# Kernel tuning notes

Hardware: AMD Instinct MI355X
Metric: run time of the kernel (lower is better)

Reference implementation:

```python
import jax, jax.numpy as jnp
import numpy as np

N_NODES = 50000
N_EDGES = 800000
IN_DIM = 128
HID = 64      # per-head out channels of conv1 (concat=False)
HID2 = 32     # hidden_dim // 2, per-head out channels of conv2
HEADS = 4
LATENT = 32
NEG_SLOPE = 0.2


def gat_conv(x, W, a_src, a_dst, bias, src, dst, n_nodes):
    """PyG GATConv with concat=False (mean over heads). src->dst message flow."""
    H, C = a_src.shape
    xh = (x @ W).reshape(-1, H, C)                       # [N,H,C]
    al_s = jnp.einsum('nhc,hc->nh', xh, a_src)           # [N,H]
    al_d = jnp.einsum('nhc,hc->nh', xh, a_dst)           # [N,H]
    alpha = jax.nn.leaky_relu(al_s[src] + al_d[dst], NEG_SLOPE)  # [E,H]
    # segment softmax over incoming edges of each dst node
    amax = jax.ops.segment_max(alpha, dst, num_segments=n_nodes)
    ex = jnp.exp(alpha - amax[dst])
    denom = jax.ops.segment_sum(ex, dst, num_segments=n_nodes)
    coef = ex / (denom[dst] + 1e-16)                     # [E,H]
    msg = xh[src] * coef[:, :, None]                     # [E,H,C]
    out = jax.ops.segment_sum(msg, dst, num_segments=n_nodes)  # [N,H,C]
    return out.mean(axis=1) + bias                       # [N,C]


def setup_inputs() -> dict:
    key = jax.random.key(0)
    ks = jax.random.split(key, 16)
    s = lambda *sh: 1.0 / np.sqrt(sh[0])
    x = jax.random.normal(ks[0], (N_NODES, IN_DIM), dtype=jnp.float32)
    edge_index = jax.random.randint(ks[1], (2, N_EDGES), 0, N_NODES, dtype=jnp.int64)
    W1 = jax.random.normal(ks[2], (IN_DIM, HEADS * HID), dtype=jnp.float32) * s(IN_DIM)
    a_src1 = jax.random.normal(ks[3], (HEADS, HID), dtype=jnp.float32) * s(HID)
    a_dst1 = jax.random.normal(ks[4], (HEADS, HID), dtype=jnp.float32) * s(HID)
    b1 = jnp.zeros((HID,), dtype=jnp.float32)
    W2 = jax.random.normal(ks[5], (HID, HEADS * HID2), dtype=jnp.float32) * s(HID)
    a_src2 = jax.random.normal(ks[6], (HEADS, HID2), dtype=jnp.float32) * s(HID2)
    a_dst2 = jax.random.normal(ks[7], (HEADS, HID2), dtype=jnp.float32) * s(HID2)
    b2 = jnp.zeros((HID2,), dtype=jnp.float32)
    W_mu = jax.random.normal(ks[8], (HID2, LATENT), dtype=jnp.float32) * s(HID2)
    b_mu = jnp.zeros((LATENT,), dtype=jnp.float32)
    W_lv = jax.random.normal(ks[9], (HID2, LATENT), dtype=jnp.float32) * s(HID2)
    b_lv = jnp.zeros((LATENT,), dtype=jnp.float32)
    return {"x": x, "edge_index": edge_index, "W1": W1, "a_src1": a_src1,
            "a_dst1": a_dst1, "b1": b1, "W2": W2, "a_src2": a_src2,
            "a_dst2": a_dst2, "b2": b2, "W_mu": W_mu, "b_mu": b_mu,
            "W_lv": W_lv, "b_lv": b_lv}


def reference(x, edge_index, W1, a_src1, a_dst1, b1, W2, a_src2, a_dst2, b2,
              W_mu, b_mu, W_lv, b_lv):
    n = x.shape[0]
    loops = jnp.arange(n, dtype=edge_index.dtype)
    src = jnp.concatenate([edge_index[0], loops])  # PyG add_self_loops=True
    dst = jnp.concatenate([edge_index[1], loops])
    h = jax.nn.relu(gat_conv(x, W1, a_src1, a_dst1, b1, src, dst, n))
    h = jax.nn.relu(gat_conv(h, W2, a_src2, a_dst2, b2, src, dst, n))
    mu = h @ W_mu + b_mu
    logvar = h @ W_lv + b_lv
    return (mu, logvar)
```

## Files before the change

kernel.cpp:

```cpp
#include <hip/hip_runtime.h>
#include <hip/hip_fp16.h>

#define N_NODES 50000
#define N_EDGES 800000
#define IN_DIM  128
#define HID     64
#define HID2    32
#define HEADS   4
#define LATENT  32
#define NEG_SLOPE 0.2f
#define BINCAP  64

#define GB1   ((N_NODES + 63) / 64)
#define NBIN  ((N_EDGES + 255) / 256)

typedef _Float16 half8v __attribute__((ext_vector_type(8)));
typedef _Float16 half4v __attribute__((ext_vector_type(4)));
typedef float    float4v __attribute__((ext_vector_type(4)));

#define OFF_XH1H  ((size_t)0)
#define OFF_XH2H  ((size_t)0)
#define OFF_ALS2  ((size_t)8000000)
#define OFF_ALD2  ((size_t)8200000)
#define OFF_AGG1  ((size_t)8400000)
#define OFF_ALS1  ((size_t)11600000)
#define OFF_ALD1  ((size_t)11800000)
#define OFF_CUR   ((size_t)12000000)
#define OFF_ESRC  ((size_t)12050000)
#define OFF_W1TH  ((size_t)15250000)
#define OFF_W2TH  ((size_t)15266384)

#define NB_ZERO ((N_NODES + 255) / 256)

__device__ __forceinline__ float lrelu(float v) {
    return v > 0.f ? v : NEG_SLOPE * v;
}

__global__ void k_prep(const float* __restrict__ W1, const float* __restrict__ W2,
                       __half* __restrict__ w1t, __half* __restrict__ w2t,
                       int* __restrict__ cur) {
    if (blockIdx.x < 160) {
        const int t = blockIdx.x * 256 + threadIdx.x;
        if (t < 32768) {
            const int k = t >> 8, n = t & 255;
            w1t[n * IN_DIM + k] = __float2half(W1[t]);
        } else {
            const int t2 = t - 32768;
            const int k = t2 >> 7, n = t2 & 127;
            w2t[n * HID + k] = __float2half(W2[t2]);
        }
    } else {
        const int i = (blockIdx.x - 160) * 256 + threadIdx.x;
        if (i < N_NODES) cur[i] = 0;
    }
}

__global__ void k_gemm1_mfma(const float* __restrict__ x, const __half* __restrict__ w1t,
                             const float* __restrict__ as1, const float* __restrict__ ad1,
                             __half* __restrict__ xh1, float* __restrict__ als,
                             float* __restrict__ ald, const int* __restrict__ ei,
                             int* __restrict__ cur, int* __restrict__ esrc) {
    const int tid = threadIdx.x;
    if (blockIdx.x >= GB1) {
        const int e = (blockIdx.x - GB1) * 256 + tid;
        if (e < N_EDGES) {
            const int s = ei[e], dd = ei[N_EDGES + e];
            const int pos = atomicAdd(&cur[dd], 1);
            if (pos < BINCAP)
                __builtin_nontemporal_store(s, &esrc[(dd << 6) + pos]);
        }
        return;
    }
    __shared__ _Float16 xsh[64][136];
    __shared__ _Float16 wsh[64][136];
    const int m0 = blockIdx.x * 64;
#pragma unroll
    for (int i = 0; i < 8; i++) {
        const int f = tid + i * 256;
        const int r = f >> 5;
        const int k = (f & 31) * 4;
        const int gr = (m0 + r < N_NODES) ? (m0 + r) : (N_NODES - 1);
        const float4 xv = *(const float4*)(x + (size_t)gr * IN_DIM + k);
        half4v hv = { (_Float16)xv.x, (_Float16)xv.y, (_Float16)xv.z, (_Float16)xv.w };
        *(half4v*)&xsh[r][k] = hv;
    }
    const int w = tid >> 6, l = tid & 63;
    const int lr = l & 15;
    const int lk = (l >> 4) * 8;
    const int rbase = m0 + w * 16 + (l >> 4) * 4;
    for (int nb = 0; nb < 4; nb++) {
        const int n0 = nb * 64;
        __syncthreads();
#pragma unroll
        for (int i = 0; i < 4; i++) {
            const int u = tid + i * 256;
            const int r = u >> 4;
            const int k = (u & 15) * 8;
            *(half8v*)&wsh[r][k] = *(const half8v*)(w1t + (size_t)(n0 + r) * IN_DIM + k);
        }
        __syncthreads();
        float4v acc0 = {0.f,0.f,0.f,0.f}, acc1 = {0.f,0.f,0.f,0.f};
        float4v acc2 = {0.f,0.f,0.f,0.f}, acc3 = {0.f,0.f,0.f,0.f};
#pragma unroll
        for (int k0 = 0; k0 < IN_DIM; k0 += 32) {
            const half8v a  = *(const half8v*)&xsh[w * 16 + lr][k0 + lk];
            const half8v b0 = *(const half8v*)&wsh[ 0 + lr][k0 + lk];
            const half8v b1 = *(const half8v*)&wsh[16 + lr][k0 + lk];
            const half8v b2 = *(const half8v*)&wsh[32 + lr][k0 + lk];
            const half8v b3 = *(const half8v*)&wsh[48 + lr][k0 + lk];
            acc0 = __builtin_amdgcn_mfma_f32_16x16x32_f16(a, b0, acc0, 0, 0, 0);
            acc1 = __builtin_amdgcn_mfma_f32_16x16x32_f16(a, b1, acc1, 0, 0, 0);
            acc2 = __builtin_amdgcn_mfma_f32_16x16x32_f16(a, b2, acc2, 0, 0, 0);
            acc3 = __builtin_amdgcn_mfma_f32_16x16x32_f16(a, b3, acc3, 0, 0, 0);
        }
        const int cbase = n0 + lr;
#pragma unroll
        for (int r = 0; r < 4; r++) {
            const int node = rbase + r;
            if (node < N_NODES) {
                __half* p = xh1 + (size_t)node * (HEADS * HID) + cbase;
                p[0]  = __float2half(acc0[r]);
                p[16] = __float2half(acc1[r]);
                p[32] = __float2half(acc2[r]);
                p[48] = __float2half(acc3[r]);
            }
        }
        const int h = nb;
        const float a0 = as1[(h << 6) + lr +  0], a1 = as1[(h << 6) + lr + 16];
        const float a2 = as1[(h << 6) + lr + 32], a3 = as1[(h << 6) + lr + 48];
        const float d0 = ad1[(h << 6) + lr +  0], d1 = ad1[(h << 6) + lr + 16];
        const float d2 = ad1[(h << 6) + lr + 32], d3 = ad1[(h << 6) + lr + 48];
#pragma unroll
        for (int r = 0; r < 4; r++) {
            float ps = acc0[r] * a0 + acc1[r] * a1 + acc2[r] * a2 + acc3[r] * a3;
            float pd = acc0[r] * d0 + acc1[r] * d1 + acc2[r] * d2 + acc3[r] * d3;
            ps += __shfl_xor(ps, 1); pd += __shfl_xor(pd, 1);
            ps += __shfl_xor(ps, 2); pd += __shfl_xor(pd, 2);
            ps += __shfl_xor(ps, 4); pd += __shfl_xor(pd, 4);
            ps += __shfl_xor(ps, 8); pd += __shfl_xor(pd, 8);
            if (lr == 0) {
                const int node = rbase + r;
                if (node < N_NODES) {
                    als[node * HEADS + h] = ps;
                    ald[node * HEADS + h] = pd;
                }
            }
        }
    }
}

__global__ void k_agg1_h(const int* __restrict__ cnt, const int* __restrict__ esrc,
                         const float* __restrict__ als, const float* __restrict__ ald,
                         const __half* __restrict__ xh1, float* __restrict__ agg1) {
    const int d = blockIdx.x * 4 + (threadIdx.x >> 6);
    const int lane = threadIdx.x & 63;
    if (d >= N_NODES) return;
    const int hq = lane >> 4;
    const int he = lane & 3;
    const float adh = ald[d * 4 + he];
    const int base = d << 6;
    const int total = cnt[d] + 1;
    float acc0 = 0.f, acc1 = 0.f, acc2 = 0.f, acc3 = 0.f;
    float denp = 0.f;
    const size_t lby = (size_t)(lane << 3);
    for (int t0 = 0; t0 < total; t0 += 16) {
        int m = total - t0; if (m > 16) m = 16;
        const int slot = lane >> 2;
        float ev = 0.f; int s = d;
        if (slot < m) {
            const int t = t0 + slot;
            if (t > 0) s = esrc[base + t - 1];
            ev = expf(lrelu(als[s * 4 + he] + adh));
        }
        denp += ev;
        int j = 0;
        for (; j + 8 <= m; j += 8) {
            int ss[8]; float cc[8]; float2 rr[8];
#pragma unroll
            for (int u = 0; u < 8; u++) ss[u] = __shfl(s, (j + u) * 4);
#pragma unroll
            for (int u = 0; u < 8; u++)
                rr[u] = *(const float2*)((const char*)xh1 + ((size_t)ss[u] << 9) + lby);
#pragma unroll
            for (int u = 0; u < 8; u++) cc[u] = __shfl(ev, (j + u) * 4 + hq);
#pragma unroll
            for (int u = 0; u < 8; u++) {
                const float2 a = __half22float2(*(const __half2*)&rr[u].x);
                const float2 b = __half22float2(*(const __half2*)&rr[u].y);
                acc0 += cc[u] * a.x; acc1 += cc[u] * a.y;
                acc2 += cc[u] * b.x; acc3 += cc[u] * b.y;
            }
        }
        for (; j + 4 <= m; j += 4) {
            int ss[4]; float cc[4]; float2 rr[4];
#pragma unroll
            for (int u = 0; u < 4; u++) ss[u] = __shfl(s, (j + u) * 4);
#pragma unroll
            for (int u = 0; u < 4; u++)
                rr[u] = *(const float2*)((const char*)xh1 + ((size_t)ss[u] << 9) + lby);
#pragma unroll
            for (int u = 0; u < 4; u++) cc[u] = __shfl(ev, (j + u) * 4 + hq);
#pragma unroll
            for (int u = 0; u < 4; u++) {
                const float2 a = __half22float2(*(const __half2*)&rr[u].x);
                const float2 b = __half22float2(*(const __half2*)&rr[u].y);
                acc0 += cc[u] * a.x; acc1 += cc[u] * a.y;
                acc2 += cc[u] * b.x; acc3 += cc[u] * b.y;
            }
        }
        for (; j < m; j++) {
            const float cf = __shfl(ev, j * 4 + hq);
            const int sj   = __shfl(s, j * 4);
            const float2 raw = *(const float2*)((const char*)xh1 + ((size_t)sj << 9) + lby);
            const float2 a = __half22float2(*(const __half2*)&raw.x);
            const float2 b = __half22float2(*(const __half2*)&raw.y);
            acc0 += cf * a.x; acc1 += cf * a.y; acc2 += cf * b.x; acc3 += cf * b.y;
        }
    }
    denp += __shfl_xor(denp, 4);
    denp += __shfl_xor(denp, 8);
    denp += __shfl_xor(denp, 16);
    denp += __shfl_xor(denp, 32);
    const float deninv = 1.f / __shfl(denp, hq);
    acc0 *= deninv; acc1 *= deninv; acc2 *= deninv; acc3 *= deninv;
    acc0 += __shfl_xor(acc0, 16); acc0 += __shfl_xor(acc0, 32);
    acc1 += __shfl_xor(acc1, 16); acc1 += __shfl_xor(acc1, 32);
    acc2 += __shfl_xor(acc2, 16); acc2 += __shfl_xor(acc2, 32);
    acc3 += __shfl_xor(acc3, 16); acc3 += __shfl_xor(acc3, 32);
    if (lane < 16) {
        float4 st = { 0.25f * acc0, 0.25f * acc1, 0.25f * acc2, 0.25f * acc3 };
        *(float4*)(agg1 + (size_t)d * HID + lane * 4) = st;
    }
}

__global__ void k_gemm2_mfma(const float* __restrict__ agg1, const float* __restrict__ b1,
                             const __half* __restrict__ w2t, const float* __restrict__ as2,
                             const float* __restrict__ ad2, __half* __restrict__ xh2,
                             float* __restrict__ als, float* __restrict__ ald) {
    __shared__ _Float16 ash[64][72];
    __shared__ _Float16 wsh[128][72];
    const int tid = threadIdx.x;
    const int m0 = blockIdx.x * 64;
#pragma unroll
    for (int i = 0; i < 4; i++) {
        const int f = tid + i * 256;
        const int r = f >> 4;
        const int k4 = (f & 15) * 4;
        const int gr = (m0 + r < N_NODES) ? (m0 + r) : (N_NODES - 1);
        float4 v = *(const float4*)(agg1 + (size_t)gr * HID + k4);
        v.x += b1[k4 + 0]; v.y += b1[k4 + 1];
        v.z += b1[k4 + 2]; v.w += b1[k4 + 3];
        v.x = v.x > 0.f ? v.x : 0.f;
        v.y = v.y > 0.f ? v.y : 0.f;
        v.z = v.z > 0.f ? v.z : 0.f;
        v.w = v.w > 0.f ? v.w : 0.f;
        half4v hv = { (_Float16)v.x, (_Float16)v.y, (_Float16)v.z, (_Float16)v.w };
        *(half4v*)&ash[r][k4] = hv;
    }
#pragma unroll
    for (int i = 0; i < 4; i++) {
        const int u = tid + i * 256;
        const int r = u >> 3;
        const int k = (u & 7) * 8;
        *(half8v*)&wsh[r][k] = *(const half8v*)(w2t + (size_t)r * HID + k);
    }
    __syncthreads();
    const int w = tid >> 6, l = tid & 63;
    const int lr = l & 15, lk = (l >> 4) * 8;
    float4v acc[8];
#pragma unroll
    for (int c = 0; c < 8; c++) acc[c] = (float4v){0.f, 0.f, 0.f, 0.f};
#pragma unroll
    for (int k0 = 0; k0 < HID; k0 += 32) {
        const half8v a = *(const half8v*)&ash[w * 16 + lr][k0 + lk];
#pragma unroll
        for (int c = 0; c < 8; c++) {
            const half8v b = *(const half8v*)&wsh[c * 16 + lr][k0 + lk];
            acc[c] = __builtin_amdgcn_mfma_f32_16x16x32_f16(a, b, acc[c], 0, 0, 0);
        }
    }
    const int rbase = m0 + w * 16 + (l >> 4) * 4;
#pragma unroll
    for (int r = 0; r < 4; r++) {
        const int node = rbase + r;
        if (node < N_NODES) {
            __half* p = xh2 + (size_t)node * (HEADS * HID2) + lr;
#pragma unroll
            for (int c = 0; c < 8; c++) p[c * 16] = __float2half(acc[c][r]);
        }
    }
    float av[8], dv[8];
#pragma unroll
    for (int c = 0; c < 8; c++) {
        const int hh = c >> 1, cih = lr + 16 * (c & 1);
        av[c] = as2[hh * HID2 + cih];
        dv[c] = ad2[hh * HID2 + cih];
    }
#pragma unroll
    for (int r = 0; r < 4; r++) {
        float ps0 = acc[0][r] * av[0] + acc[1][r] * av[1];
        float ps1 = acc[2][r] * av[2] + acc[3][r] * av[3];
        float ps2 = acc[4][r] * av[4] + acc[5][r] * av[5];
        float ps3 = acc[6][r] * av[6] + acc[7][r] * av[7];
        float pd0 = acc[0][r] * dv[0] + acc[1][r] * dv[1];
        float pd1 = acc[2][r] * dv[2] + acc[3][r] * dv[3];
        float pd2 = acc[4][r] * dv[4] + acc[5][r] * dv[5];
        float pd3 = acc[6][r] * dv[6] + acc[7][r] * dv[7];
#pragma unroll
        for (int off = 1; off <= 8; off <<= 1) {
            ps0 += __shfl_xor(ps0, off); ps1 += __shfl_xor(ps1, off);
            ps2 += __shfl_xor(ps2, off); ps3 += __shfl_xor(ps3, off);
            pd0 += __shfl_xor(pd0, off); pd1 += __shfl_xor(pd1, off);
            pd2 += __shfl_xor(pd2, off); pd3 += __shfl_xor(pd3, off);
        }
        if (lr == 0) {
            const int node = rbase + r;
            if (node < N_NODES) {
                float4 sv = { ps0, ps1, ps2, ps3 };
                float4 dvv = { pd0, pd1, pd2, pd3 };
                *(float4*)(als + (size_t)node * HEADS) = sv;
                *(float4*)(ald + (size_t)node * HEADS) = dvv;
            }
        }
    }
}

__global__ void k_agg2_final(const int* __restrict__ cnt, const int* __restrict__ esrc,
                             const float* __restrict__ als, const float* __restrict__ ald,
                             const __half* __restrict__ xh2, const float* __restrict__ b2,
                             const float* __restrict__ Wmu, const float* __restrict__ bmu,
                             const float* __restrict__ Wlv, const float* __restrict__ blv,
                             float* __restrict__ out) {
    const int d = blockIdx.x * 4 + (threadIdx.x >> 6);
    const int lane = threadIdx.x & 63;
    if (d >= N_NODES) return;
    const int hq = lane >> 4;
    const int he = lane & 3;
    const float adh = ald[d * 4 + he];
    const int base = d << 6;
    const int total = cnt[d] + 1;
    float acc0 = 0.f, acc1 = 0.f;
    float denp = 0.f;
    const size_t lby = (size_t)(lane << 2);
    for (int t0 = 0; t0 < total; t0 += 16) {
        int m = total - t0; if (m > 16) m = 16;
        const int slot = lane >> 2;
        float ev = 0.f; int s = d;
        if (slot < m) {
            const int t = t0 + slot;
            if (t > 0) s = esrc[base + t - 1];
            ev = expf(lrelu(als[s * 4 + he] + adh));
        }
        denp += ev;
        int j = 0;
        for (; j + 8 <= m; j += 8) {
            int ss[8]; float cc[8]; __half2 rr[8];
#pragma unroll
            for (int u = 0; u < 8; u++) ss[u] = __shfl(s, (j + u) * 4);
#pragma unroll
            for (int u = 0; u < 8; u++)
                rr[u] = *(const __half2*)((const char*)xh2 + ((size_t)ss[u] << 8) + lby);
#pragma unroll
            for (int u = 0; u < 8; u++) cc[u] = __shfl(ev, (j + u) * 4 + hq);
#pragma unroll
            for (int u = 0; u < 8; u++) {
                const float2 xv = __half22float2(rr[u]);
                acc0 += cc[u] * xv.x; acc1 += cc[u] * xv.y;
            }
        }
        for (; j + 4 <= m; j += 4) {
            int ss[4]; float cc[4]; __half2 rr[4];
#pragma unroll
            for (int u = 0; u < 4; u++) ss[u] = __shfl(s, (j + u) * 4);
#pragma unroll
            for (int u = 0; u < 4; u++)
                rr[u] = *(const __half2*)((const char*)xh2 + ((size_t)ss[u] << 8) + lby);
#pragma unroll
            for (int u = 0; u < 4; u++) cc[u] = __shfl(ev, (j + u) * 4 + hq);
#pragma unroll
            for (int u = 0; u < 4; u++) {
                const float2 xv = __half22float2(rr[u]);
                acc0 += cc[u] * xv.x; acc1 += cc[u] * xv.y;
            }
        }
        for (; j < m; j++) {
            const float cf = __shfl(ev, j * 4 + hq);
            const int sj   = __shfl(s, j * 4);
            const __half2 hv = *(const __half2*)((const char*)xh2 + ((size_t)sj << 8) + lby);
            const float2 xv = __half22float2(hv);
            acc0 += cf * xv.x; acc1 += cf * xv.y;
        }
    }
    denp += __shfl_xor(denp, 4);
    denp += __shfl_xor(denp, 8);
    denp += __shfl_xor(denp, 16);
    denp += __shfl_xor(denp, 32);
    const float deninv = 1.f / __shfl(denp, hq);
    acc0 *= deninv; acc1 *= deninv;
    acc0 += __shfl_xor(acc0, 16); acc0 += __shfl_xor(acc0, 32);
    acc1 += __shfl_xor(acc1, 16); acc1 += __shfl_xor(acc1, 32);
    const int cp = lane & 15;
    float h0 = 0.25f * acc0 + b2[2 * cp];
    float h1 = 0.25f * acc1 + b2[2 * cp + 1];
    h0 = h0 > 0.f ? h0 : 0.f;
    h1 = h1 > 0.f ? h1 : 0.f;
    const int jj = lane & 31;
    const bool lv = lane >= 32;
    const float* Wp = lv ? Wlv : Wmu;
    const float* bp = lv ? blv : bmu;
    float o = bp[jj];
#pragma unroll
    for (int k = 0; k < 16; k++) {
        const float e0 = __shfl(h0, k);
        const float e1 = __shfl(h1, k);
        o += e0 * Wp[(2 * k) * LATENT + jj] + e1 * Wp[(2 * k + 1) * LATENT + jj];
    }
    out[(lv ? (size_t)N_NODES * LATENT : (size_t)0) + (size_t)d * LATENT + jj] = o;
}

extern "C" void kernel_launch(void* const* d_in, const int* in_sizes, int n_in,
                              void* d_out, int out_size, void* d_ws, size_t ws_size,
                              hipStream_t stream) {
    const float* x    = (const float*)d_in[0];
    const int*   ei   = (const int*)d_in[1];
    const float* W1   = (const float*)d_in[2];
    const float* as1  = (const float*)d_in[3];
    const float* ad1  = (const float*)d_in[4];
    const float* b1   = (const float*)d_in[5];
    const float* W2   = (const float*)d_in[6];
    const float* as2  = (const float*)d_in[7];
    const float* ad2  = (const float*)d_in[8];
    const float* b2   = (const float*)d_in[9];
    const float* Wmu  = (const float*)d_in[10];
    const float* bmu  = (const float*)d_in[11];
    const float* Wlv  = (const float*)d_in[12];
    const float* blv  = (const float*)d_in[13];
    float* out = (float*)d_out;
    float* ws  = (float*)d_ws;

    __half* xh1h = (__half*)(ws + OFF_XH1H);
    __half* xh2h = (__half*)(ws + OFF_XH2H);
    __half* w1th = (__half*)(ws + OFF_W1TH);
    __half* w2th = (__half*)(ws + OFF_W2TH);
    float* als1 = ws + OFF_ALS1;
    float* ald1 = ws + OFF_ALD1;
    float* agg1 = ws + OFF_AGG1;
    float* als2 = ws + OFF_ALS2;
    float* ald2 = ws + OFF_ALD2;
    int* cur  = (int*)(ws + OFF_CUR);
    int* esrc = (int*)(ws + OFF_ESRC);

    k_prep<<<160 + NB_ZERO, 256, 0, stream>>>(W1, W2, w1th, w2th, cur);

    k_gemm1_mfma<<<GB1 + NBIN, 256, 0, stream>>>(x, w1th, as1, ad1, xh1h,
                                                 als1, ald1, ei, cur, esrc);

    k_agg1_h<<<(N_NODES + 3) / 4, 256, 0, stream>>>(cur, esrc, als1, ald1, xh1h, agg1);

    k_gemm2_mfma<<<(N_NODES + 63) / 64, 256, 0, stream>>>(agg1, b1, w2th, as2, ad2,
                                                          xh2h, als2, ald2);

    k_agg2_final<<<(N_NODES + 3) / 4, 256, 0, stream>>>(cur, esrc, als2, ald2, xh2h,
                                                        b2, Wmu, bmu, Wlv, blv, out);
}
```

Measured before the change: 202.5 us.

## Split per-node edge bins into sub-bins with 16-bit source indices

The destination-binning step now spreads each node's counter over 8 sub-bins selected by edge index, and stores source ids as 16-bit values in fixed-capacity sub-slots. The two aggregation kernels rebuild a prefix over the sub-bin counts and map each edge slot back to its sub-bin with a small compare-and-select routine. Binning blocks are also moved ahead of the GEMM blocks in the fused launch so they get scheduled first. The goal is less atomic contention on the counters and less index traffic. In exchange the aggregation loop does more integer ALU work per edge, and 16-bit ids only hold while node count stays below 65536.

```diff
diff --git a/kernel.cpp b/kernel.cpp
--- a/kernel.cpp
+++ b/kernel.cpp
@@ -9,7 +9,9 @@
 #define HEADS   4
 #define LATENT  32
 #define NEG_SLOPE 0.2f
-#define BINCAP  64
+#define SUBBINS 8
+#define SUBCAP  20
+#define ROWSLOT (SUBBINS * SUBCAP)
 
 #define GB1   ((N_NODES + 63) / 64)
 #define NBIN  ((N_EDGES + 255) / 256)
@@ -26,11 +28,11 @@
 #define OFF_ALS1  ((size_t)11600000)
 #define OFF_ALD1  ((size_t)11800000)
 #define OFF_CUR   ((size_t)12000000)
-#define OFF_ESRC  ((size_t)12050000)
-#define OFF_W1TH  ((size_t)15250000)
-#define OFF_W2TH  ((size_t)15266384)
-
-#define NB_ZERO ((N_NODES + 255) / 256)
+#define OFF_ESRC  ((size_t)12400000)
+#define OFF_W1TH  ((size_t)16400000)
+#define OFF_W2TH  ((size_t)16416384)
+
+#define NB_ZERO ((N_NODES * SUBBINS + 255) / 256)
 
 __device__ __forceinline__ float lrelu(float v) {
     return v > 0.f ? v : NEG_SLOPE * v;
@@ -51,7 +53,7 @@
         }
     } else {
         const int i = (blockIdx.x - 160) * 256 + threadIdx.x;
-        if (i < N_NODES) cur[i] = 0;
+        if (i < N_NODES * SUBBINS) cur[i] = 0;
     }
 }
 
@@ -59,21 +61,22 @@
                              const float* __restrict__ as1, const float* __restrict__ ad1,
                              __half* __restrict__ xh1, float* __restrict__ als,
                              float* __restrict__ ald, const int* __restrict__ ei,
-                             int* __restrict__ cur, int* __restrict__ esrc) {
+                             int* __restrict__ cur, unsigned short* __restrict__ esrc) {
     const int tid = threadIdx.x;
-    if (blockIdx.x >= GB1) {
-        const int e = (blockIdx.x - GB1) * 256 + tid;
+    if (blockIdx.x < NBIN) {
+        const int e = blockIdx.x * 256 + tid;
         if (e < N_EDGES) {
             const int s = ei[e], dd = ei[N_EDGES + e];
-            const int pos = atomicAdd(&cur[dd], 1);
-            if (pos < BINCAP)
-                __builtin_nontemporal_store(s, &esrc[(dd << 6) + pos]);
+            const int sub = e & (SUBBINS - 1);
+            const int pos = atomicAdd(&cur[dd * SUBBINS + sub], 1);
+            if (pos < SUBCAP)
+                esrc[(size_t)dd * ROWSLOT + sub * SUBCAP + pos] = (unsigned short)s;
         }
         return;
     }
     __shared__ _Float16 xsh[64][136];
     __shared__ _Float16 wsh[64][136];
-    const int m0 = blockIdx.x * 64;
+    const int m0 = (blockIdx.x - NBIN) * 64;
 #pragma unroll
     for (int i = 0; i < 8; i++) {
         const int f = tid + i * 256;
@@ -149,7 +152,21 @@
     }
 }
 
-__global__ void k_agg1_h(const int* __restrict__ cnt, const int* __restrict__ esrc,
+__device__ __forceinline__ int bin_slot(int u, int p1, int p2, int p3, int p4,
+                                        int p5, int p6, int p7) {
+    const int b = (u >= p1) + (u >= p2) + (u >= p3) + (u >= p4) +
+                  (u >= p5) + (u >= p6) + (u >= p7);
+    int pb = (b >= 1) ? p1 : 0;
+    pb = (b >= 2) ? p2 : pb;
+    pb = (b >= 3) ? p3 : pb;
+    pb = (b >= 4) ? p4 : pb;
+    pb = (b >= 5) ? p5 : pb;
+    pb = (b >= 6) ? p6 : pb;
+    pb = (b >= 7) ? p7 : pb;
+    return b * SUBCAP + (u - pb);
+}
+
+__global__ void k_agg1_h(const int* __restrict__ cnt, const unsigned short* __restrict__ esrc,
                          const float* __restrict__ als, const float* __restrict__ ald,
                          const __half* __restrict__ xh1, float* __restrict__ agg1) {
     const int d = blockIdx.x * 4 + (threadIdx.x >> 6);
@@ -158,8 +175,12 @@
     const int hq = lane >> 4;
     const int he = lane & 3;
     const float adh = ald[d * 4 + he];
-    const int base = d << 6;
-    const int total = cnt[d] + 1;
+    const int4 c0 = *(const int4*)(cnt + d * SUBBINS);
+    const int4 c1 = *(const int4*)(cnt + d * SUBBINS + 4);
+    const int p1 = c0.x, p2 = p1 + c0.y, p3 = p2 + c0.z, p4 = p3 + c0.w;
+    const int p5 = p4 + c1.x, p6 = p5 + c1.y, p7 = p6 + c1.z, p8 = p7 + c1.w;
+    const int total = p8 + 1;
+    const unsigned short* erow = esrc + (size_t)d * ROWSLOT;
     float acc0 = 0.f, acc1 = 0.f, acc2 = 0.f, acc3 = 0.f;
     float denp = 0.f;
     const size_t lby = (size_t)(lane << 3);
@@ -169,7 +190,7 @@
         float ev = 0.f; int s = d;
         if (slot < m) {
             const int t = t0 + slot;
-            if (t > 0) s = esrc[base + t - 1];
+            if (t > 0) s = erow[bin_slot(t - 1, p1, p2, p3, p4, p5, p6, p7)];
             ev = expf(lrelu(als[s * 4 + he] + adh));
         }
         denp += ev;
@@ -325,7 +346,7 @@
     }
 }
 
-__global__ void k_agg2_final(const int* __restrict__ cnt, const int* __restrict__ esrc,
+__global__ void k_agg2_final(const int* __restrict__ cnt, const unsigned short* __restrict__ esrc,
                              const float* __restrict__ als, const float* __restrict__ ald,
                              const __half* __restrict__ xh2, const float* __restrict__ b2,
                              const float* __restrict__ Wmu, const float* __restrict__ bmu,
@@ -337,8 +358,12 @@
     const int hq = lane >> 4;
     const int he = lane & 3;
     const float adh = ald[d * 4 + he];
-    const int base = d << 6;
-    const int total = cnt[d] + 1;
+    const int4 c0 = *(const int4*)(cnt + d * SUBBINS);
+    const int4 c1 = *(const int4*)(cnt + d * SUBBINS + 4);
+    const int p1 = c0.x, p2 = p1 + c0.y, p3 = p2 + c0.z, p4 = p3 + c0.w;
+    const int p5 = p4 + c1.x, p6 = p5 + c1.y, p7 = p6 + c1.z, p8 = p7 + c1.w;
+    const int total = p8 + 1;
+    const unsigned short* erow = esrc + (size_t)d * ROWSLOT;
     float acc0 = 0.f, acc1 = 0.f;
     float denp = 0.f;
     const size_t lby = (size_t)(lane << 2);
@@ -348,7 +373,7 @@
         float ev = 0.f; int s = d;
         if (slot < m) {
             const int t = t0 + slot;
-            if (t > 0) s = esrc[base + t - 1];
+            if (t > 0) s = erow[bin_slot(t - 1, p1, p2, p3, p4, p5, p6, p7)];
             ev = expf(lrelu(als[s * 4 + he] + adh));
         }
         denp += ev;
@@ -448,11 +473,11 @@
     float* als2 = ws + OFF_ALS2;
     float* ald2 = ws + OFF_ALD2;
     int* cur  = (int*)(ws + OFF_CUR);
-    int* esrc = (int*)(ws + OFF_ESRC);
+    unsigned short* esrc = (unsigned short*)(ws + OFF_ESRC);
 
     k_prep<<<160 + NB_ZERO, 256, 0, stream>>>(W1, W2, w1th, w2th, cur);
 
-    k_gemm1_mfma<<<GB1 + NBIN, 256, 0, stream>>>(x, w1th, as1, ad1, xh1h,
+    k_gemm1_mfma<<<NBIN + GB1, 256, 0, stream>>>(x, w1th, as1, ad1, xh1h,
                                                  als1, ald1, ei, cur, esrc);
 
     k_agg1_h<<<(N_NODES + 3) / 4, 256, 0, stream>>>(cur, esrc, als1, ald1, xh1h, agg1);
```

Result: slower. 213.2 us (+5.3%).
